# Kernel optimization log

Hardware: AMD Instinct MI355X
Metric: run time of the kernel (lower is better)

Reference implementation:

```python
import jax, jax.numpy as jnp
import numpy as np

N_BLOCKS = 5
D_HIDDEN = 512
D_LATENT = 512
NUM_FREQ = 10
IMG_H = IMG_W = 128


@jax.custom_vjp
def trunc_exp(x):
    return jnp.exp(x)

def _te_fwd(x):
    return jnp.exp(x), x

def _te_bwd(x, g):
    return (g * jnp.exp(jnp.clip(x, -15.0, 15.0)),)

trunc_exp.defvjp(_te_fwd, _te_bwd)


def setup_inputs() -> dict:
    key = jax.random.key(0)
    ks = jax.random.split(key, 12)
    cam, ray, samp = 2, 1024, 48
    world_xyz = jax.random.normal(ks[0], (cam, ray, samp, 3), jnp.float32) * 0.5
    world_xyz = world_xyz.at[..., 2].add(2.5)  # keep points in front of identity camera
    c2w = jnp.tile(jnp.eye(4, dtype=jnp.float32), (cam, 1, 1))
    k_mat = jnp.tile(jnp.array([[128.0, 0.0, 64.0], [0.0, 128.0, 64.0], [0.0, 0.0, 1.0]], jnp.float32), (cam, 1, 1))
    features = jax.random.normal(ks[1], (cam, D_LATENT, IMG_H, IMG_W), jnp.float32)
    s = 0.02
    d_in = 3 + 3 * 2 * NUM_FREQ  # 63
    return {
        'world_xyz': world_xyz,
        'c2w': c2w,
        'k_mat': k_mat,
        'features': features,
        'lin_in_w': jax.random.normal(ks[2], (d_in, D_HIDDEN), jnp.float32) * s,
        'lin_in_b': jnp.zeros((D_HIDDEN,), jnp.float32),
        'lin_z_w': jax.random.normal(ks[3], (N_BLOCKS, D_LATENT, D_HIDDEN), jnp.float32) * s,
        'lin_z_b': jnp.zeros((N_BLOCKS, D_HIDDEN), jnp.float32),
        'fc0_w': jax.random.normal(ks[4], (N_BLOCKS, D_HIDDEN, D_HIDDEN), jnp.float32) * s,
        'fc0_b': jnp.zeros((N_BLOCKS, D_HIDDEN), jnp.float32),
        'fc1_w': jax.random.normal(ks[5], (N_BLOCKS, D_HIDDEN, D_HIDDEN), jnp.float32) * s,
        'fc1_b': jnp.zeros((N_BLOCKS, D_HIDDEN), jnp.float32),
        'lin_out_w': jax.random.normal(ks[6], (D_HIDDEN, 1), jnp.float32) * s,
        'lin_out_b': jnp.zeros((1,), jnp.float32),
    }


def _bilinear(feat, uv):
    # feat: [C, H, W]; uv: [N, 2] pixel coords. Bilinear, border padding, align_corners=True.
    Hd, Wd = feat.shape[1], feat.shape[2]
    x = jnp.clip(uv[:, 0], 0.0, Wd - 1.0)
    y = jnp.clip(uv[:, 1], 0.0, Hd - 1.0)
    x0 = jnp.floor(x); y0 = jnp.floor(y)
    x0i = x0.astype(jnp.int32); y0i = y0.astype(jnp.int32)
    x1i = jnp.minimum(x0i + 1, Wd - 1); y1i = jnp.minimum(y0i + 1, Hd - 1)
    wx = x - x0; wy = y - y0
    f00 = feat[:, y0i, x0i]; f01 = feat[:, y0i, x1i]
    f10 = feat[:, y1i, x0i]; f11 = feat[:, y1i, x1i]
    out = (f00 * ((1 - wx) * (1 - wy)) + f01 * (wx * (1 - wy)) +
           f10 * ((1 - wx) * wy) + f11 * (wx * wy))
    return out.T  # [N, C]


def _forward(world_xyz, c2w, k_mat, features, lin_in_w, lin_in_b, lin_z_w, lin_z_b,
             fc0_w, fc0_b, fc1_w, fc1_b, lin_out_w, lin_out_b):
    B, R, S, _ = world_xyz.shape
    pts = world_xyz.reshape(B, R * S, 3)
    # world -> camera (w2c = inverse of rigid c2w)
    rot = c2w[:, :3, :3]
    trans = c2w[:, :3, 3]
    cam_xyz = jnp.einsum('bji,bnj->bni', rot, pts - trans[:, None])  # R^T (p - t)
    # project with intrinsics
    uvw = jnp.einsum('bij,bnj->bni', k_mat, cam_xyz)
    z = uvw[..., 2:3]
    z = jnp.where(jnp.abs(z) < 1e-6, 1e-6, z)
    uv = uvw[..., :2] / z  # [B, N, 2] pixel coords
    aligned = jax.vmap(_bilinear)(features, uv)  # [B, N, C]
    # NeRF positional encoding (include_input=True, freqs 2^0..2^9, scaled by 2*pi)
    freqs = 2.0 ** jnp.arange(NUM_FREQ, dtype=jnp.float32)
    scaled = (2.0 * jnp.pi) * cam_xyz[..., None] * freqs  # [B, N, 3, F]
    scaled = scaled.reshape(B, R * S, 3 * NUM_FREQ)
    enc = jnp.concatenate([cam_xyz, jnp.sin(scaled), jnp.cos(scaled)], axis=-1)  # [B, N, 63]
    # ResnetFC: lin_in then residual blocks with latent injection
    h = enc @ lin_in_w + lin_in_b
    for i in range(N_BLOCKS):
        h = h + aligned @ lin_z_w[i] + lin_z_b[i]
        net = jax.nn.relu(h) @ fc0_w[i] + fc0_b[i]
        dx = jax.nn.relu(net) @ fc1_w[i] + fc1_b[i]
        h = h + dx
    sigma = jax.nn.relu(h) @ lin_out_w + lin_out_b  # [B, N, 1]
    return trunc_exp(sigma).reshape(B, R, S, 1)


def reference(world_xyz, c2w, k_mat, features, lin_in_w, lin_in_b, lin_z_w, lin_z_b,
              fc0_w, fc0_b, fc1_w, fc1_b, lin_out_w, lin_out_b):
    return _forward(world_xyz, c2w, k_mat, features, lin_in_w, lin_in_b, lin_z_w, lin_z_b,
                    fc0_w, fc0_b, fc1_w, fc1_b, lin_out_w, lin_out_b)
```

## Files before the change

kernel.cpp:

```cpp
#include <hip/hip_runtime.h>

typedef __bf16 bf16_t;
typedef bf16_t bf16x8 __attribute__((ext_vector_type(8)));
typedef float f32x4 __attribute__((ext_vector_type(4)));
typedef unsigned short u16;

#define P_TOTAL 98304
#define PTS_PER_BATCH 49152
#define PITCH 520

__device__ __forceinline__ u16 f2bs(float f){ bf16_t b=(bf16_t)f; return __builtin_bit_cast(u16,b); }

__global__ void k_wtrans15(const float* __restrict__ lz, const float* __restrict__ f0,
                           const float* __restrict__ f1, u16* __restrict__ dst){
  int kt = blockIdx.x, ns = blockIdx.y, z = blockIdx.z;
  const float* src = (z<5) ? (lz + (size_t)z*262144)
                   : (z<10 ? (f0 + (size_t)(z-5)*262144)
                           : (f1 + (size_t)(z-10)*262144));
  u16* d = dst + (size_t)z*262144 + (size_t)(ns*16 + kt)*1024;
  int l = threadIdx.x;
  int col = ns*32 + (l&15);
  int kr  = kt*32 + (l>>4)*8;
  #pragma unroll
  for (int nt=0;nt<2;nt++){
    bf16x8 o;
    #pragma unroll
    for (int j=0;j<8;j++) o[j] = (bf16_t)src[(size_t)(kr+j)*512 + col + nt*16];
    *(bf16x8*)(d + nt*512 + l*8) = o;
  }
}

__global__ void k_wtrans_in(const float* __restrict__ w, u16* __restrict__ dst){
  int kt = blockIdx.x, ns = blockIdx.y;
  u16* d = dst + (size_t)(ns*2 + kt)*1024;
  int l = threadIdx.x;
  int col = ns*32 + (l&15);
  int kr  = kt*32 + (l>>4)*8;
  #pragma unroll
  for (int nt=0;nt<2;nt++){
    bf16x8 o;
    #pragma unroll
    for (int j=0;j<8;j++){
      int k = kr + j;
      o[j] = (k < 63) ? (bf16_t)w[(size_t)k*512 + col + nt*16] : (bf16_t)0.f;
    }
    *(bf16x8*)(d + nt*512 + l*8) = o;
  }
}

__global__ void k_featT(const float* __restrict__ feat, u16* __restrict__ featT){
  int x = threadIdx.x;
  int c8 = blockIdx.x*8;
  int y = blockIdx.y, b = blockIdx.z;
  float v[8];
  #pragma unroll
  for (int j=0;j<8;j++)
    v[j] = feat[(((size_t)(b*512 + c8 + j))*128 + y)*128 + x];
  bf16x8 o;
  #pragma unroll
  for (int j=0;j<8;j++) o[j] = (bf16_t)v[j];
  *(bf16x8*)(featT + (((size_t)(b*128 + y))*128 + x)*512 + c8) = o;
}

__global__ void k_points(const float* __restrict__ world, const float* __restrict__ c2w,
                         const float* __restrict__ kmat, const u16* __restrict__ featT,
                         u16* __restrict__ alignedB, u16* __restrict__ encB){
  int wid = threadIdx.x >> 6, lane = threadIdx.x & 63;
  int gp = blockIdx.x*4 + wid;
  int b = gp / PTS_PER_BATCH;
  const float* wp = world + (size_t)gp*3;
  float px = wp[0], py = wp[1], pz = wp[2];
  const float* cw = c2w + b*16;
  float dx = px - cw[3], dy = py - cw[7], dz = pz - cw[11];
  float cx = cw[0]*dx + cw[4]*dy + cw[8]*dz;
  float cy = cw[1]*dx + cw[5]*dy + cw[9]*dz;
  float cz = cw[2]*dx + cw[6]*dy + cw[10]*dz;
  const float* km = kmat + b*9;
  float u0 = km[0]*cx + km[1]*cy + km[2]*cz;
  float v0 = km[3]*cx + km[4]*cy + km[5]*cz;
  float zz = km[6]*cx + km[7]*cy + km[8]*cz;
  if (fabsf(zz) < 1e-6f) zz = 1e-6f;
  float uu = u0/zz, vv = v0/zz;
  float xf = fminf(fmaxf(uu, 0.f), 127.f);
  float yf = fminf(fmaxf(vv, 0.f), 127.f);
  float x0f = floorf(xf), y0f = floorf(yf);
  int x0 = (int)x0f, y0 = (int)y0f;
  int x1 = min(x0+1,127), y1 = min(y0+1,127);
  float wx = xf - x0f, wy = yf - y0f;
  float w00 = (1.f-wx)*(1.f-wy), w01 = wx*(1.f-wy), w10 = (1.f-wx)*wy, w11 = wx*wy;
  size_t fb = (size_t)b*128*128*512;
  int c8 = lane*8;
  const bf16x8 t00 = *(const bf16x8*)(featT + fb + (size_t)(y0*128+x0)*512 + c8);
  const bf16x8 t01 = *(const bf16x8*)(featT + fb + (size_t)(y0*128+x1)*512 + c8);
  const bf16x8 t10 = *(const bf16x8*)(featT + fb + (size_t)(y1*128+x0)*512 + c8);
  const bf16x8 t11 = *(const bf16x8*)(featT + fb + (size_t)(y1*128+x1)*512 + c8);
  bf16x8 o;
  #pragma unroll
  for (int j=0;j<8;j++){
    float r = (float)t00[j]*w00 + (float)t01[j]*w01 + (float)t10[j]*w10 + (float)t11[j]*w11;
    o[j] = (bf16_t)r;
  }
  *(bf16x8*)(alignedB + (size_t)gp*512 + c8) = o;
  float cam[3] = {cx, cy, cz};
  float e;
  if (lane < 3) e = cam[lane];
  else if (lane < 33){
    int i = (lane-3)/10, f = (lane-3)%10;
    e = sinf(6.2831855f * cam[i] * (float)(1<<f));
  } else if (lane < 63){
    int i = (lane-33)/10, f = (lane-33)%10;
    e = cosf(6.2831855f * cam[i] * (float)(1<<f));
  } else e = 0.f;
  encB[(size_t)gp*64 + lane] = f2bs(e);
}


template<int NK>
__device__ __forceinline__ void gemm2(const u16* sB, const u16* __restrict__ Af,
                                      int fm, int fk8, int l, f32x4 (&acc)[4][4]){
  const u16* ap = Af + l*8;
  constexpr int NS = NK*1024;
  bf16x8 a[2][4];
  #pragma unroll
  for (int d=0; d<2; ++d)
    #pragma unroll
    for (int nt=0; nt<4; ++nt)
      a[d][nt] = *(const bf16x8*)(ap + (nt>>1)*NS + d*1024 + (nt&1)*512);
  const u16* bp = sB + fm*PITCH + fk8*8;
  #pragma unroll 1
  for (int kb=0; kb<NK/2-1; ++kb){
    #pragma unroll
    for (int d=0; d<2; ++d){
      const int kt = kb*2 + d;
      bf16x8 bfr[4];
      #pragma unroll
      for (int bt=0; bt<4; ++bt)
        bfr[bt] = *(const bf16x8*)(bp + bt*16*PITCH + kt*32);
      bf16x8 a0 = a[d][0], a1 = a[d][1], a2 = a[d][2], a3 = a[d][3];
      #pragma unroll
      for (int nt=0; nt<4; ++nt)
        a[d][nt] = *(const bf16x8*)(ap + (nt>>1)*NS + (kt+2)*1024 + (nt&1)*512);
      #pragma unroll
      for (int bt=0; bt<4; ++bt){
        acc[bt][0] = __builtin_amdgcn_mfma_f32_16x16x32_bf16(a0, bfr[bt], acc[bt][0], 0,0,0);
        acc[bt][1] = __builtin_amdgcn_mfma_f32_16x16x32_bf16(a1, bfr[bt], acc[bt][1], 0,0,0);
        acc[bt][2] = __builtin_amdgcn_mfma_f32_16x16x32_bf16(a2, bfr[bt], acc[bt][2], 0,0,0);
        acc[bt][3] = __builtin_amdgcn_mfma_f32_16x16x32_bf16(a3, bfr[bt], acc[bt][3], 0,0,0);
      }
    }
  }
  #pragma unroll
  for (int d=0; d<2; ++d){
    const int kt = NK - 2 + d;
    bf16x8 bfr[4];
    #pragma unroll
    for (int bt=0; bt<4; ++bt)
      bfr[bt] = *(const bf16x8*)(bp + bt*16*PITCH + kt*32);
    #pragma unroll
    for (int bt=0; bt<4; ++bt)
      #pragma unroll
      for (int nt=0; nt<4; ++nt)
        acc[bt][nt] = __builtin_amdgcn_mfma_f32_16x16x32_bf16(a[d][nt], bfr[bt], acc[bt][nt], 0,0,0);
  }
}

__device__ __forceinline__ void add_bias2(const float* __restrict__ bias, int wn64, int rq,
                                          f32x4 (&acc)[4][4]){
  #pragma unroll
  for (int nt=0; nt<4; ++nt){
    f32x4 bv = *(const f32x4*)&bias[wn64 + nt*16 + rq];
    #pragma unroll
    for (int bt=0; bt<4; ++bt)
      #pragma unroll
      for (int r=0; r<4; ++r)
        acc[bt][nt][r] += bv[r];
  }
}

__device__ __forceinline__ void write_relu2(u16* dst, int fm, int rq, int wn64,
                                            f32x4 (&acc)[4][4]){
  #pragma unroll
  for (int bt=0; bt<4; ++bt){
    int m = bt*16 + fm;
    #pragma unroll
    for (int nt=0; nt<4; ++nt){
      int kb = wn64 + nt*16 + rq;
      u16 p0 = f2bs(fmaxf(acc[bt][nt][0], 0.f));
      u16 p1 = f2bs(fmaxf(acc[bt][nt][1], 0.f));
      u16 p2 = f2bs(fmaxf(acc[bt][nt][2], 0.f));
      u16 p3 = f2bs(fmaxf(acc[bt][nt][3], 0.f));
      uint2 v;
      v.x = (unsigned)p0 | ((unsigned)p1 << 16);
      v.y = (unsigned)p2 | ((unsigned)p3 << 16);
      *(uint2*)&dst[m*PITCH + kb] = v;
    }
  }
}

__global__ __launch_bounds__(512, 2) void k_net(
    const u16* __restrict__ alignedB, const u16* __restrict__ encB,
    const u16* __restrict__ wtin, const float* __restrict__ b_in,
    const u16* __restrict__ wts, const float* __restrict__ bz,
    const float* __restrict__ b0, const float* __restrict__ b1,
    const float* __restrict__ wout, const float* __restrict__ bout,
    float* __restrict__ out)
{
  __shared__ u16 bufA[64*PITCH];
  __shared__ u16 bufB[64*PITCH];
  const int t = threadIdx.x, w = t>>6, l = t&63;
  const int m0 = blockIdx.x*64;
  const int wn64 = w*64, fm = l&15, fk8 = l>>4, rq = (l>>4)*4;

  {
    int m = t>>3, c = t&7;
    #pragma unroll
    for (int j=0;j<8;j++){
      int kc = c + j*8;
      *(uint4*)&bufA[m*PITCH + kc*8] =
          *(const uint4*)(alignedB + (size_t)(m0+m)*512 + kc*8);
    }
  }
  {
    int m = t>>3, kc = t&7;
    *(uint4*)&bufB[m*PITCH + kc*8] =
        *(const uint4*)(encB + (size_t)(m0+m)*64 + kc*8);
  }
  __syncthreads();

  f32x4 h[4][4] = {};
  gemm2<2>(bufB, wtin + (size_t)w*4096, fm, fk8, l, h);
  add_bias2(b_in, wn64, rq, h);

  #pragma unroll 1
  for (int i=0;i<5;i++){
    gemm2<16>(bufA, wts + (size_t)i*262144 + (size_t)w*32768, fm, fk8, l, h);
    add_bias2(bz + i*512, wn64, rq, h);
    __syncthreads();
    write_relu2(bufB, fm, rq, wn64, h);
    __syncthreads();
    f32x4 acc[4][4] = {};
    gemm2<16>(bufB, wts + (size_t)(5+i)*262144 + (size_t)w*32768, fm, fk8, l, acc);
    add_bias2(b0 + i*512, wn64, rq, acc);
    __syncthreads();
    write_relu2(bufB, fm, rq, wn64, acc);
    __syncthreads();
    gemm2<16>(bufB, wts + (size_t)(10+i)*262144 + (size_t)w*32768, fm, fk8, l, h);
    add_bias2(b1 + i*512, wn64, rq, h);
  }

  float s[4];
  {
    #pragma unroll
    for (int bt=0; bt<4; ++bt) s[bt] = 0.f;
    #pragma unroll
    for (int nt=0; nt<4; ++nt){
      f32x4 wv = *(const f32x4*)&wout[wn64 + nt*16 + rq];
      #pragma unroll
      for (int bt=0; bt<4; ++bt)
        #pragma unroll
        for (int r=0; r<4; ++r)
          s[bt] += fmaxf(h[bt][nt][r], 0.f) * wv[r];
    }
  }
  #pragma unroll
  for (int bt=0; bt<4; ++bt){
    s[bt] += __shfl_xor(s[bt], 16, 64);
    s[bt] += __shfl_xor(s[bt], 32, 64);
  }
  __syncthreads();
  float* red = (float*)bufB;
  if (l < 16){
    #pragma unroll
    for (int bt=0; bt<4; ++bt)
      red[w*64 + bt*16 + l] = s[bt];
  }
  __syncthreads();
  if (t < 64){
    float a = bout[0];
    #pragma unroll
    for (int wv=0; wv<8; wv++) a += red[wv*64 + t];
    out[m0 + t] = expf(a);
  }
}

extern "C" void kernel_launch(void* const* d_in, const int* in_sizes, int n_in,
                              void* d_out, int out_size, void* d_ws, size_t ws_size,
                              hipStream_t stream) {
  const float* world = (const float*)d_in[0];
  const float* c2w   = (const float*)d_in[1];
  const float* kmat  = (const float*)d_in[2];
  const float* feat  = (const float*)d_in[3];
  const float* w_in  = (const float*)d_in[4];
  const float* b_in  = (const float*)d_in[5];
  const float* w_z   = (const float*)d_in[6];
  const float* b_z   = (const float*)d_in[7];
  const float* w_f0  = (const float*)d_in[8];
  const float* b_f0  = (const float*)d_in[9];
  const float* w_f1  = (const float*)d_in[10];
  const float* b_f1  = (const float*)d_in[11];
  const float* w_out = (const float*)d_in[12];
  const float* b_out = (const float*)d_in[13];
  float* out = (float*)d_out;
  char* ws = (char*)d_ws;

  size_t off = 0;
  u16* wts   = (u16*)(ws + off); off += (size_t)15*262144*2;
  u16* wtin  = (u16*)(ws + off); off += (size_t)512*64*2;
  u16* featT = (u16*)(ws + off); off += (size_t)2*128*128*512*2;
  u16* alignedB = (u16*)(ws + off); off += (size_t)P_TOTAL*512*2;
  u16* encB  = (u16*)(ws + off); off += (size_t)P_TOTAL*64*2;

  k_wtrans15<<<dim3(16,16,15), 64, 0, stream>>>(w_z, w_f0, w_f1, wts);
  k_wtrans_in<<<dim3(2,16,1), 64, 0, stream>>>(w_in, wtin);
  k_featT<<<dim3(64,128,2), 128, 0, stream>>>(feat, featT);
  k_points<<<dim3(P_TOTAL/4), 256, 0, stream>>>(world, c2w, kmat, featT, alignedB, encB);
  k_net<<<dim3(P_TOTAL/64), 512, 0, stream>>>(alignedB, encB, wtin, b_in, wts,
      b_z, b_f0, b_f1, w_out, b_out, out);
}
```

Before: 851.9 us.

## Prefetch next GEMM weights across stages and double-buffer LDS operand loads

```diff
diff --git a/kernel.cpp b/kernel.cpp
--- a/kernel.cpp
+++ b/kernel.cpp
@@ -10,6 +10,12 @@
 #define PITCH 520
 
 __device__ __forceinline__ u16 f2bs(float f){ bf16_t b=(bf16_t)f; return __builtin_bit_cast(u16,b); }
+
+__device__ __forceinline__ void bar_lds(){
+  asm volatile("s_waitcnt lgkmcnt(0)" ::: "memory");
+  __builtin_amdgcn_s_barrier();
+  __builtin_amdgcn_sched_barrier(0);
+}
 
 __global__ void k_wtrans15(const float* __restrict__ lz, const float* __restrict__ f0,
                            const float* __restrict__ f1, u16* __restrict__ dst){
@@ -115,52 +121,55 @@
 }
 
 
+#define MFMA_BF16 __builtin_amdgcn_mfma_f32_16x16x32_bf16
+
 template<int NK>
-__device__ __forceinline__ void gemm2(const u16* sB, const u16* __restrict__ Af,
-                                      int fm, int fk8, int l, f32x4 (&acc)[4][4]){
-  const u16* ap = Af + l*8;
-  constexpr int NS = NK*1024;
-  bf16x8 a[2][4];
-  #pragma unroll
-  for (int d=0; d<2; ++d)
-    #pragma unroll
-    for (int nt=0; nt<4; ++nt)
-      a[d][nt] = *(const bf16x8*)(ap + (nt>>1)*NS + d*1024 + (nt&1)*512);
+__device__ __forceinline__ void gemm2(const u16* sB, const u16* __restrict__ apS,
+                                      const u16* __restrict__ apN,
+                                      int fm, int fk8, f32x4 (&acc)[4][4], bf16x8 (&a)[2][4]){
   const u16* bp = sB + fm*PITCH + fk8*8;
+  bf16x8 br[2][4];
+  #pragma unroll
+  for (int bt=0; bt<4; ++bt) br[0][bt] = *(const bf16x8*)(bp + bt*16*PITCH);
   #pragma unroll 1
   for (int kb=0; kb<NK/2-1; ++kb){
     #pragma unroll
     for (int d=0; d<2; ++d){
       const int kt = kb*2 + d;
-      bf16x8 bfr[4];
       #pragma unroll
       for (int bt=0; bt<4; ++bt)
-        bfr[bt] = *(const bf16x8*)(bp + bt*16*PITCH + kt*32);
-      bf16x8 a0 = a[d][0], a1 = a[d][1], a2 = a[d][2], a3 = a[d][3];
+        br[d^1][bt] = *(const bf16x8*)(bp + bt*16*PITCH + (kt+1)*32);
+      bf16x8 ac0=a[d][0], ac1=a[d][1], ac2=a[d][2], ac3=a[d][3];
       #pragma unroll
       for (int nt=0; nt<4; ++nt)
-        a[d][nt] = *(const bf16x8*)(ap + (nt>>1)*NS + (kt+2)*1024 + (nt&1)*512);
+        a[d][nt] = *(const bf16x8*)(apS + (nt>>1)*(NK*1024) + (kt+2)*1024 + (nt&1)*512);
       #pragma unroll
       for (int bt=0; bt<4; ++bt){
-        acc[bt][0] = __builtin_amdgcn_mfma_f32_16x16x32_bf16(a0, bfr[bt], acc[bt][0], 0,0,0);
-        acc[bt][1] = __builtin_amdgcn_mfma_f32_16x16x32_bf16(a1, bfr[bt], acc[bt][1], 0,0,0);
-        acc[bt][2] = __builtin_amdgcn_mfma_f32_16x16x32_bf16(a2, bfr[bt], acc[bt][2], 0,0,0);
-        acc[bt][3] = __builtin_amdgcn_mfma_f32_16x16x32_bf16(a3, bfr[bt], acc[bt][3], 0,0,0);
+        acc[bt][0] = MFMA_BF16(ac0, br[d][bt], acc[bt][0], 0,0,0);
+        acc[bt][1] = MFMA_BF16(ac1, br[d][bt], acc[bt][1], 0,0,0);
+        acc[bt][2] = MFMA_BF16(ac2, br[d][bt], acc[bt][2], 0,0,0);
+        acc[bt][3] = MFMA_BF16(ac3, br[d][bt], acc[bt][3], 0,0,0);
       }
     }
   }
   #pragma unroll
   for (int d=0; d<2; ++d){
-    const int kt = NK - 2 + d;
-    bf16x8 bfr[4];
-    #pragma unroll
-    for (int bt=0; bt<4; ++bt)
-      bfr[bt] = *(const bf16x8*)(bp + bt*16*PITCH + kt*32);
-    #pragma unroll
-    for (int bt=0; bt<4; ++bt)
-      #pragma unroll
-      for (int nt=0; nt<4; ++nt)
-        acc[bt][nt] = __builtin_amdgcn_mfma_f32_16x16x32_bf16(a[d][nt], bfr[bt], acc[bt][nt], 0,0,0);
+    if (d == 0){
+      #pragma unroll
+      for (int bt=0; bt<4; ++bt)
+        br[1][bt] = *(const bf16x8*)(bp + bt*16*PITCH + (NK-1)*32);
+    }
+    bf16x8 ac0=a[d][0], ac1=a[d][1], ac2=a[d][2], ac3=a[d][3];
+    #pragma unroll
+    for (int nt=0; nt<4; ++nt)
+      a[d][nt] = *(const bf16x8*)(apN + (nt>>1)*16384 + d*1024 + (nt&1)*512);
+    #pragma unroll
+    for (int bt=0; bt<4; ++bt){
+      acc[bt][0] = MFMA_BF16(ac0, br[d][bt], acc[bt][0], 0,0,0);
+      acc[bt][1] = MFMA_BF16(ac1, br[d][bt], acc[bt][1], 0,0,0);
+      acc[bt][2] = MFMA_BF16(ac2, br[d][bt], acc[bt][2], 0,0,0);
+      acc[bt][3] = MFMA_BF16(ac3, br[d][bt], acc[bt][3], 0,0,0);
+    }
   }
 }
 
@@ -211,6 +220,14 @@
   const int m0 = blockIdx.x*64;
   const int wn64 = w*64, fm = l&15, fk8 = l>>4, rq = (l>>4)*4;
 
+  const u16* apE = wtin + (size_t)w*4096 + l*8;
+  bf16x8 afr[2][4];
+  #pragma unroll
+  for (int d=0; d<2; ++d)
+    #pragma unroll
+    for (int nt=0; nt<4; ++nt)
+      afr[d][nt] = *(const bf16x8*)(apE + (nt>>1)*2048 + d*1024 + (nt&1)*512);
+
   {
     int m = t>>3, c = t&7;
     #pragma unroll
@@ -225,26 +242,32 @@
     *(uint4*)&bufB[m*PITCH + kc*8] =
         *(const uint4*)(encB + (size_t)(m0+m)*64 + kc*8);
   }
-  __syncthreads();
-
+  bar_lds();
+
+  const u16* apz0 = wts + (size_t)w*32768 + l*8;
   f32x4 h[4][4] = {};
-  gemm2<2>(bufB, wtin + (size_t)w*4096, fm, fk8, l, h);
+  gemm2<2>(bufB, apE, apz0, fm, fk8, h, afr);
   add_bias2(b_in, wn64, rq, h);
 
   #pragma unroll 1
   for (int i=0;i<5;i++){
-    gemm2<16>(bufA, wts + (size_t)i*262144 + (size_t)w*32768, fm, fk8, l, h);
+    const u16* apz  = wts + (size_t)i*262144      + (size_t)w*32768 + l*8;
+    const u16* apf0 = wts + (size_t)(5+i)*262144  + (size_t)w*32768 + l*8;
+    const u16* apf1 = wts + (size_t)(10+i)*262144 + (size_t)w*32768 + l*8;
+    const u16* apzn = (i<4) ? (wts + (size_t)(i+1)*262144 + (size_t)w*32768 + l*8) : apE;
+
+    gemm2<16>(bufA, apz, apf0, fm, fk8, h, afr);
     add_bias2(bz + i*512, wn64, rq, h);
-    __syncthreads();
+    bar_lds();
     write_relu2(bufB, fm, rq, wn64, h);
-    __syncthreads();
+    bar_lds();
     f32x4 acc[4][4] = {};
-    gemm2<16>(bufB, wts + (size_t)(5+i)*262144 + (size_t)w*32768, fm, fk8, l, acc);
+    gemm2<16>(bufB, apf0, apf1, fm, fk8, acc, afr);
     add_bias2(b0 + i*512, wn64, rq, acc);
-    __syncthreads();
+    bar_lds();
     write_relu2(bufB, fm, rq, wn64, acc);
-    __syncthreads();
-    gemm2<16>(bufB, wts + (size_t)(10+i)*262144 + (size_t)w*32768, fm, fk8, l, h);
+    bar_lds();
+    gemm2<16>(bufB, apf1, apzn, fm, fk8, h, afr);
     add_bias2(b1 + i*512, wn64, rq, h);
   }
 
@@ -267,14 +290,14 @@
     s[bt] += __shfl_xor(s[bt], 16, 64);
     s[bt] += __shfl_xor(s[bt], 32, 64);
   }
-  __syncthreads();
+  bar_lds();
   float* red = (float*)bufB;
   if (l < 16){
     #pragma unroll
     for (int bt=0; bt<4; ++bt)
       red[w*64 + bt*16 + l] = s[bt];
   }
-  __syncthreads();
+  bar_lds();
   if (t < 64){
     float a = bout[0];
     #pragma unroll
```

Measured after the change: 837.3 us. Within noise of the previous version (-1.7%).
